# Kernel optimization log

Hardware: AMD Instinct MI355X
Metric: run time of the kernel (lower is better)

The kernel has to match this reference:

```python
import jax, jax.numpy as jnp
import numpy as np

BN_EPS = 1e-5


def sparsemax(z):
    # z: [B, D]; sparse projection onto the simplex along last axis.
    D = z.shape[-1]
    z_sorted = jnp.flip(jnp.sort(z, axis=-1), axis=-1)          # descending
    cs = jnp.cumsum(z_sorted, axis=-1)                           # cumulative sums
    k = jnp.arange(1, D + 1, dtype=z.dtype)                      # 1..D
    support = (1.0 + k * z_sorted) > cs                          # support condition
    k_star = jnp.sum(support, axis=-1, keepdims=True)            # support size, int
    cs_k = jnp.take_along_axis(cs, k_star - 1, axis=-1)
    tau = (cs_k - 1.0) / k_star.astype(z.dtype)                  # threshold
    return jnp.maximum(z - tau, 0.0)


def setup_inputs() -> dict:
    key = jax.random.key(0)
    k1, k2, k3 = jax.random.split(key, 3)
    B, D = 32768, 1024
    a = jax.random.normal(k1, (B, D), dtype=jnp.float32)
    p = jax.random.uniform(k2, (B, D), dtype=jnp.float32)        # prior scales in (0,1)
    W = jax.random.normal(k3, (D, D), dtype=jnp.float32) * (1.0 / np.sqrt(D))
    b = jnp.zeros((D,), dtype=jnp.float32)
    gamma = jnp.ones((D,), dtype=jnp.float32)
    beta = jnp.zeros((D,), dtype=jnp.float32)
    return {"a": a, "p": p, "W": W, "b": b, "gamma": gamma, "beta": beta}


def reference(a, p, W, b, gamma, beta):
    # Linear: a @ W^T + b  (torch nn.Linear convention)
    h = jnp.einsum("bd,ed->be", a, W) + b
    # BatchNorm1d (training mode: batch stats, biased variance)
    mean = jnp.mean(h, axis=0)
    var = jnp.mean(jnp.square(h - mean), axis=0)
    h = (h - mean) * jax.lax.rsqrt(var + BN_EPS) * gamma + beta
    # Prior scaling, then sparsemax -> attention mask
    mask = sparsemax(p * h)
    return mask
```

## Files before the change

### kernel.cpp

```cpp
#include <hip/hip_runtime.h>
#include <hip/hip_fp16.h>
#include <stdint.h>

typedef _Float16 f16x8 __attribute__((ext_vector_type(8)));
typedef _Float16 f16x2 __attribute__((ext_vector_type(2)));
typedef float f32x4 __attribute__((ext_vector_type(4)));

#define BM 128
#define BN 128
#define BK 64

__device__ __forceinline__ void async_copy16(const void* g, void* l) {
  __builtin_amdgcn_global_load_lds(
      (__attribute__((address_space(1))) void*)(g),
      (__attribute__((address_space(3))) void*)(l),
      16, 0, 0);
}

__global__ __launch_bounds__(256) void cvt_f32_f16_2(const float* __restrict__ inA, size_t na,
                                                     const float* __restrict__ inW, size_t nw,
                                                     _Float16* __restrict__ outA,
                                                     _Float16* __restrict__ outW) {
  size_t i = ((size_t)blockIdx.x * 256 + threadIdx.x) * 8;
  const float* in;
  _Float16* out;
  if (i < na) {
    in = inA; out = outA;
  } else {
    i -= na;
    if (i >= nw) return;
    in = inW; out = outW;
  }
  float4 u = *(const float4*)(in + i);
  float4 v = *(const float4*)(in + i + 4);
  f16x8 h;
  h[0] = (_Float16)u.x; h[1] = (_Float16)u.y; h[2] = (_Float16)u.z; h[3] = (_Float16)u.w;
  h[4] = (_Float16)v.x; h[5] = (_Float16)v.y; h[6] = (_Float16)v.z; h[7] = (_Float16)v.w;
  *(f16x8*)(out + i) = h;
}

template <bool H16>
__global__ __launch_bounds__(256) void gemm_direct(const _Float16* __restrict__ Ah,
                                                   const _Float16* __restrict__ Wh,
                                                   const float* __restrict__ bias,
                                                   void* __restrict__ Hout,
                                                   float* __restrict__ psum,
                                                   float* __restrict__ psumsq,
                                                   int M, int N, int K) {
  __shared__ __attribute__((aligned(16))) _Float16 lsA[BM * BK];
  __shared__ __attribute__((aligned(16))) _Float16 lsB[BN * BK];

  const int tid  = threadIdx.x;
  const int wave = tid >> 6;
  const int lane = tid & 63;
  const int wrow = (wave >> 1) * 64;
  const int wcol = (wave & 1) * 64;
  const int l16  = lane & 15;
  const int quad = lane >> 4;

  const int nx = gridDim.x;
  const int li = blockIdx.y * nx + blockIdx.x;
  const int xcd = li & 7;
  const int jj  = li >> 3;
  const int bnT = jj % nx;
  const int bmT = xcd + (jj / nx) * 8;
  const int bm = bmT * BM;
  const int bn = bnT * BN;

  f32x4 acc[4][4];
#pragma unroll
  for (int i = 0; i < 4; ++i)
#pragma unroll
    for (int j = 0; j < 4; ++j) acc[i][j] = (f32x4){0.f, 0.f, 0.f, 0.f};

  for (int k0 = 0; k0 < K; k0 += BK) {
#pragma unroll
    for (int i = 0; i < 4; ++i) {
      const int basechunk = i * 256 + wave * 64;
      const int g   = basechunk + lane;
      const int row = g >> 3;
      const int kc  = ((g & 7) ^ (row & 7)) << 3;
      async_copy16(Ah + (size_t)(bm + row) * K + k0 + kc, &lsA[basechunk * 8]);
      async_copy16(Wh + (size_t)(bn + row) * K + k0 + kc, &lsB[basechunk * 8]);
    }
    __syncthreads();

#pragma unroll
    for (int kk = 0; kk < BK; kk += 32) {
      f16x8 af[4], bf[4];
#pragma unroll
      for (int i = 0; i < 4; ++i) {
        const int r = wrow + i * 16 + l16;
        const int col = ((kk >> 3) + quad) ^ (l16 & 7);
        af[i] = *(const f16x8*)&lsA[r * 64 + col * 8];
      }
#pragma unroll
      for (int j = 0; j < 4; ++j) {
        const int r = wcol + j * 16 + l16;
        const int col = ((kk >> 3) + quad) ^ (l16 & 7);
        bf[j] = *(const f16x8*)&lsB[r * 64 + col * 8];
      }
#pragma unroll
      for (int i = 0; i < 4; ++i)
#pragma unroll
        for (int j = 0; j < 4; ++j)
          acc[i][j] = __builtin_amdgcn_mfma_f32_16x16x32_f16(af[i], bf[j], acc[i][j], 0, 0, 0);
    }
    __syncthreads();
  }

#pragma unroll
  for (int j = 0; j < 4; ++j) {
    const int c = bn + wcol + j * 16 + l16;
    const float bv = bias[c];
    float s = 0.f, s2 = 0.f;
#pragma unroll
    for (int i = 0; i < 4; ++i) {
      const int r = bm + wrow + i * 16 + quad * 4;
      f32x4 v = acc[i][j];
      const float v0 = v[0] + bv, v1 = v[1] + bv, v2 = v[2] + bv, v3 = v[3] + bv;
      s += v0 + v1 + v2 + v3;
      s2 += v0 * v0 + v1 * v1 + v2 * v2 + v3 * v3;
      if constexpr (H16) {
        f16x2* H2 = (f16x2*)Hout;
        const size_t d0 = (size_t)(r >> 1) * N + c;
        H2[d0]     = (f16x2){(_Float16)v0, (_Float16)v1};
        H2[d0 + N] = (f16x2){(_Float16)v2, (_Float16)v3};
      } else {
        float* Cp = (float*)Hout + (size_t)r * N + c;
        Cp[0] = v0; Cp[(size_t)N] = v1; Cp[2 * (size_t)N] = v2; Cp[3 * (size_t)N] = v3;
      }
    }
    s  += __shfl_xor(s, 16, 64);  s  += __shfl_xor(s, 32, 64);
    s2 += __shfl_xor(s2, 16, 64); s2 += __shfl_xor(s2, 32, 64);
    if (quad == 0) {
      const size_t slot = (size_t)(bmT * 2 + (wave >> 1)) * N + c;
      psum[slot] = s;
      psumsq[slot] = s2;
    }
  }
}

__global__ __launch_bounds__(256) void gemm_fallback(const float* __restrict__ Af,
                                                     const float* __restrict__ Wf,
                                                     const float* __restrict__ bias,
                                                     float* __restrict__ C,
                                                     float* __restrict__ sum,
                                                     float* __restrict__ sumsq,
                                                     int M, int N, int K) {
  __shared__ __attribute__((aligned(16))) _Float16 lsA[BM * BK];
  __shared__ __attribute__((aligned(16))) _Float16 lsB[BN * BK];
  const int tid  = threadIdx.x;
  const int wave = tid >> 6;
  const int lane = tid & 63;
  const int wrow = (wave >> 1) * 64;
  const int wcol = (wave & 1) * 64;
  const int l16  = lane & 15;
  const int quad = lane >> 4;
  const int bm = blockIdx.y * BM;
  const int bn = blockIdx.x * BN;

  f32x4 acc[4][4];
#pragma unroll
  for (int i = 0; i < 4; ++i)
#pragma unroll
    for (int j = 0; j < 4; ++j) acc[i][j] = (f32x4){0.f, 0.f, 0.f, 0.f};

  for (int k0 = 0; k0 < K; k0 += BK) {
#pragma unroll
    for (int i = 0; i < 4; ++i) {
      const int g   = i * 256 + tid;
      const int row = g >> 3;
      const int kc  = ((g & 7) ^ (row & 7)) << 3;
      {
        const float* src = Af + (size_t)(bm + row) * K + k0 + kc;
        float4 u = *(const float4*)src;
        float4 v = *(const float4*)(src + 4);
        f16x8 h;
        h[0] = (_Float16)u.x; h[1] = (_Float16)u.y; h[2] = (_Float16)u.z; h[3] = (_Float16)u.w;
        h[4] = (_Float16)v.x; h[5] = (_Float16)v.y; h[6] = (_Float16)v.z; h[7] = (_Float16)v.w;
        *(f16x8*)&lsA[g * 8] = h;
      }
      {
        const float* src = Wf + (size_t)(bn + row) * K + k0 + kc;
        float4 u = *(const float4*)src;
        float4 v = *(const float4*)(src + 4);
        f16x8 h;
        h[0] = (_Float16)u.x; h[1] = (_Float16)u.y; h[2] = (_Float16)u.z; h[3] = (_Float16)u.w;
        h[4] = (_Float16)v.x; h[5] = (_Float16)v.y; h[6] = (_Float16)v.z; h[7] = (_Float16)v.w;
        *(f16x8*)&lsB[g * 8] = h;
      }
    }
    __syncthreads();
#pragma unroll
    for (int kk = 0; kk < BK; kk += 32) {
      f16x8 af[4], bf[4];
#pragma unroll
      for (int i = 0; i < 4; ++i) {
        const int r = wrow + i * 16 + l16;
        const int col = ((kk >> 3) + quad) ^ (l16 & 7);
        af[i] = *(const f16x8*)&lsA[r * 64 + col * 8];
      }
#pragma unroll
      for (int j = 0; j < 4; ++j) {
        const int r = wcol + j * 16 + l16;
        const int col = ((kk >> 3) + quad) ^ (l16 & 7);
        bf[j] = *(const f16x8*)&lsB[r * 64 + col * 8];
      }
#pragma unroll
      for (int i = 0; i < 4; ++i)
#pragma unroll
        for (int j = 0; j < 4; ++j)
          acc[i][j] = __builtin_amdgcn_mfma_f32_16x16x32_f16(af[i], bf[j], acc[i][j], 0, 0, 0);
    }
    __syncthreads();
  }

#pragma unroll
  for (int j = 0; j < 4; ++j) {
    const int c = bn + wcol + j * 16 + l16;
    const float bv = bias[c];
    float s = 0.f, s2 = 0.f;
#pragma unroll
    for (int i = 0; i < 4; ++i) {
      const int r = bm + wrow + i * 16 + quad * 4;
      float* Cp = C + (size_t)r * N + c;
      f32x4 v = acc[i][j];
#pragma unroll
      for (int rr = 0; rr < 4; ++rr) {
        float val = v[rr] + bv;
        Cp[(size_t)rr * N] = val;
        s += val;
        s2 += val * val;
      }
    }
    s  += __shfl_xor(s, 16, 64);  s  += __shfl_xor(s, 32, 64);
    s2 += __shfl_xor(s2, 16, 64); s2 += __shfl_xor(s2, 32, 64);
    if (quad == 0) {
      atomicAdd(&sum[c], s);
      atomicAdd(&sumsq[c], s2);
    }
  }
}

__global__ __launch_bounds__(256) void bn_finalize_wave(const float* __restrict__ psum,
                                                        const float* __restrict__ psumsq,
                                                        const float* __restrict__ gamma,
                                                        const float* __restrict__ beta,
                                                        float* __restrict__ scale,
                                                        float* __restrict__ shift,
                                                        float invB, int S, int D) {
  const int wave = threadIdx.x >> 6;
  const int lane = threadIdx.x & 63;
  const int c = blockIdx.x * 4 + wave;
  float s = 0.f, q = 0.f;
  for (int u = lane; u < S; u += 64) {
    s += psum[(size_t)u * D + c];
    q += psumsq[(size_t)u * D + c];
  }
#pragma unroll
  for (int o = 32; o > 0; o >>= 1) {
    s += __shfl_xor(s, o, 64);
    q += __shfl_xor(q, o, 64);
  }
  if (lane == 0) {
    float mean = s * invB;
    float var  = q * invB - mean * mean;
    float rstd = rsqrtf(var + 1e-5f);
    float sc = rstd * gamma[c];
    scale[c] = sc;
    shift[c] = beta[c] - mean * sc;
  }
}

__global__ __launch_bounds__(256) void bn_finalize(const float* __restrict__ sum,
                                                   const float* __restrict__ sumsq,
                                                   const float* __restrict__ gamma,
                                                   const float* __restrict__ beta,
                                                   float* __restrict__ scale,
                                                   float* __restrict__ shift,
                                                   float invB) {
  const int c = blockIdx.x * 256 + threadIdx.x;
  float mean = sum[c] * invB;
  float var  = sumsq[c] * invB - mean * mean;
  float rstd = rsqrtf(var + 1e-5f);
  float sc = rstd * gamma[c];
  scale[c] = sc;
  shift[c] = beta[c] - mean * sc;
}

__global__ __launch_bounds__(256) void bn_sparsemax_h2(const _Float16* __restrict__ H2,
                                                       const float* __restrict__ P,
                                                       const float* __restrict__ scale,
                                                       const float* __restrict__ shift,
                                                       float* __restrict__ out, int D) {
  const int wave = threadIdx.x >> 6;
  const int lane = threadIdx.x & 63;
  const int row = blockIdx.x * 4 + wave;
  const int rp  = row >> 1;
  const int par = row & 1;

  const f16x8* Hc = (const f16x8*)(H2 + (size_t)rp * 2 * D);
  const f32x4* P4 = (const f32x4*)(P + (size_t)row * D);
  const f32x4* SC = (const f32x4*)scale;
  const f32x4* SH = (const f32x4*)shift;

  f32x4 z[4];
  float tot = 0.f;
#pragma unroll
  for (int j = 0; j < 4; ++j) {
    const int idx = j * 64 + lane;
    f16x8 h = Hc[idx];
    f32x4 hv = {(float)h[par], (float)h[2 + par], (float)h[4 + par], (float)h[6 + par]};
    f32x4 zz = P4[idx] * (hv * SC[idx] + SH[idx]);
    z[j] = zz;
    tot += zz[0] + zz[1] + zz[2] + zz[3];
  }
#pragma unroll
  for (int o = 32; o > 0; o >>= 1) tot += __shfl_xor(tot, o, 64);

  float tau = (tot - 1.0f) / (float)D;
  float kprev = -1.0f;
  for (int it = 0; it < 64; ++it) {
    float s = 0.f, kf = 0.f;
#pragma unroll
    for (int j = 0; j < 4; ++j)
#pragma unroll
      for (int c = 0; c < 4; ++c) {
        float zz = z[j][c];
        if (zz > tau) { s += zz; kf += 1.0f; }
      }
#pragma unroll
    for (int o = 32; o > 0; o >>= 1) {
      s  += __shfl_xor(s, o, 64);
      kf += __shfl_xor(kf, o, 64);
    }
    tau = (s - 1.0f) / kf;
    if (kf == kprev) break;
    kprev = kf;
  }

  f32x4* O4 = (f32x4*)(out + (size_t)row * D);
#pragma unroll
  for (int j = 0; j < 4; ++j) {
    const int idx = j * 64 + lane;
    f32x4 o;
#pragma unroll
    for (int c = 0; c < 4; ++c) o[c] = fmaxf(z[j][c] - tau, 0.f);
    O4[idx] = o;
  }
}

__global__ __launch_bounds__(256) void bn_sparsemax_f32(const float* __restrict__ H,
                                                        const float* __restrict__ P,
                                                        const float* __restrict__ scale,
                                                        const float* __restrict__ shift,
                                                        float* __restrict__ out, int D) {
  const int wave = threadIdx.x >> 6;
  const int lane = threadIdx.x & 63;
  const int row = blockIdx.x * 4 + wave;
  const size_t rowoff = (size_t)row * D;
  const f32x4* H4 = (const f32x4*)(H + rowoff);
  const f32x4* P4 = (const f32x4*)(P + rowoff);
  const f32x4* SC = (const f32x4*)scale;
  const f32x4* SH = (const f32x4*)shift;

  f32x4 z[4];
  float tot = 0.f;
#pragma unroll
  for (int j = 0; j < 4; ++j) {
    const int idx = j * 64 + lane;
    f32x4 zz = P4[idx] * (H4[idx] * SC[idx] + SH[idx]);
    z[j] = zz;
    tot += zz[0] + zz[1] + zz[2] + zz[3];
  }
#pragma unroll
  for (int o = 32; o > 0; o >>= 1) tot += __shfl_xor(tot, o, 64);

  float tau = (tot - 1.0f) / (float)D;
  float kprev = -1.0f;
  for (int it = 0; it < 64; ++it) {
    float s = 0.f, kf = 0.f;
#pragma unroll
    for (int j = 0; j < 4; ++j)
#pragma unroll
      for (int c = 0; c < 4; ++c) {
        float zz = z[j][c];
        if (zz > tau) { s += zz; kf += 1.0f; }
      }
#pragma unroll
    for (int o = 32; o > 0; o >>= 1) {
      s  += __shfl_xor(s, o, 64);
      kf += __shfl_xor(kf, o, 64);
    }
    tau = (s - 1.0f) / kf;
    if (kf == kprev) break;
    kprev = kf;
  }

  f32x4* O4 = (f32x4*)(out + rowoff);
#pragma unroll
  for (int j = 0; j < 4; ++j) {
    const int idx = j * 64 + lane;
    f32x4 o;
#pragma unroll
    for (int c = 0; c < 4; ++c) o[c] = fmaxf(z[j][c] - tau, 0.f);
    O4[idx] = o;
  }
}

extern "C" void kernel_launch(void* const* d_in, const int* in_sizes, int n_in,
                              void* d_out, int out_size, void* d_ws, size_t ws_size,
                              hipStream_t stream) {
  const float* a     = (const float*)d_in[0];
  const float* p     = (const float*)d_in[1];
  const float* W     = (const float*)d_in[2];
  const float* b     = (const float*)d_in[3];
  const float* gamma = (const float*)d_in[4];
  const float* beta  = (const float*)d_in[5];
  float* out = (float*)d_out;

  const int D = in_sizes[3];
  const int Brows = in_sizes[0] / D;
  const int K = D, N = D;
  const size_t na = (size_t)Brows * D;
  const size_t nw = (size_t)D * D;
  const int S = (Brows / BM) * 2;

  const size_t statsB = (size_t)D * S * sizeof(float);
  float* psum   = (float*)d_ws;
  float* psumsq = (float*)((char*)d_ws + statsB);
  float* wscale = (float*)((char*)d_ws + 2 * statsB);
  float* wshift = wscale + D;
  const size_t off_Ah = 2 * statsB + 16384;
  _Float16* Ah = (_Float16*)((char*)d_ws + off_Ah);
  _Float16* Wh = Ah + na;
  _Float16* H2 = Wh + nw;
  const size_t need1 = off_Ah + (na + nw) * sizeof(_Float16);
  const size_t need2 = need1 + na * sizeof(_Float16);

  if (ws_size >= need1) {
    cvt_f32_f16_2<<<dim3((unsigned)((na + nw) / 8 / 256)), 256, 0, stream>>>(
        a, na, W, nw, Ah, Wh);
    const bool h16 = ws_size >= need2;
    if (h16) {
      gemm_direct<true><<<dim3(N / BN, Brows / BM), 256, 0, stream>>>(
          Ah, Wh, b, H2, psum, psumsq, Brows, N, K);
    } else {
      gemm_direct<false><<<dim3(N / BN, Brows / BM), 256, 0, stream>>>(
          Ah, Wh, b, out, psum, psumsq, Brows, N, K);
    }
    bn_finalize_wave<<<dim3(D / 4), 256, 0, stream>>>(psum, psumsq, gamma, beta,
                                                      wscale, wshift,
                                                      1.0f / (float)Brows, S, D);
    if (h16) {
      bn_sparsemax_h2<<<dim3(Brows / 4), 256, 0, stream>>>(H2, p, wscale, wshift, out, D);
    } else {
      bn_sparsemax_f32<<<dim3(Brows / 4), 256, 0, stream>>>(out, p, wscale, wshift, out, D);
    }
  } else {
    float* wsum   = (float*)d_ws;
    float* wsumsq = wsum + D;
    float* fscale = wsum + 2 * D;
    float* fshift = wsum + 3 * D;
    hipMemsetAsync(d_ws, 0, 2 * D * sizeof(float), stream);
    gemm_fallback<<<dim3(N / BN, Brows / BM), 256, 0, stream>>>(
        a, W, b, out, wsum, wsumsq, Brows, N, K);
    bn_finalize<<<dim3(D / 256), 256, 0, stream>>>(wsum, wsumsq, gamma, beta, fscale, fshift,
                                                   1.0f / (float)Brows);
    bn_sparsemax_f32<<<dim3(Brows / 4), 256, 0, stream>>>(out, p, fscale, fshift, out, D);
  }
}
```

Measured before the change: 424.0 us.

## Fuse activation fp32-to-fp16 conversion into GEMM tile loads, convert only weights

The separate conversion pass over the large activation matrix is removed. The GEMM now reads fp32 activations directly, converts them in registers and stores them to the swizzled LDS layout, while weights are still pre-converted and loaded asynchronously. This avoids writing and re-reading a 64MB fp16 copy of the activations. In exchange, the activation tile loads are synchronous register round-trips instead of async global-to-LDS copies, and the GEMM reads twice the bytes for A. The fallback kernel's LDS store is also changed from a swizzled global read to a swizzled LDS write.

```diff
diff --git a/kernel.cpp b/kernel.cpp
--- a/kernel.cpp
+++ b/kernel.cpp
@@ -17,20 +17,11 @@
       16, 0, 0);
 }
 
-__global__ __launch_bounds__(256) void cvt_f32_f16_2(const float* __restrict__ inA, size_t na,
-                                                     const float* __restrict__ inW, size_t nw,
-                                                     _Float16* __restrict__ outA,
-                                                     _Float16* __restrict__ outW) {
+__global__ __launch_bounds__(256) void cvt_f32_f16(const float* __restrict__ in,
+                                                   _Float16* __restrict__ out,
+                                                   size_t n) {
   size_t i = ((size_t)blockIdx.x * 256 + threadIdx.x) * 8;
-  const float* in;
-  _Float16* out;
-  if (i < na) {
-    in = inA; out = outA;
-  } else {
-    i -= na;
-    if (i >= nw) return;
-    in = inW; out = outW;
-  }
+  if (i + 8 > n) return;
   float4 u = *(const float4*)(in + i);
   float4 v = *(const float4*)(in + i + 4);
   f16x8 h;
@@ -40,13 +31,13 @@
 }
 
 template <bool H16>
-__global__ __launch_bounds__(256) void gemm_direct(const _Float16* __restrict__ Ah,
-                                                   const _Float16* __restrict__ Wh,
-                                                   const float* __restrict__ bias,
-                                                   void* __restrict__ Hout,
-                                                   float* __restrict__ psum,
-                                                   float* __restrict__ psumsq,
-                                                   int M, int N, int K) {
+__global__ __launch_bounds__(256) void gemm_a32(const float* __restrict__ Af,
+                                                const _Float16* __restrict__ Wh,
+                                                const float* __restrict__ bias,
+                                                void* __restrict__ Hout,
+                                                float* __restrict__ psum,
+                                                float* __restrict__ psumsq,
+                                                int M, int N, int K) {
   __shared__ __attribute__((aligned(16))) _Float16 lsA[BM * BK];
   __shared__ __attribute__((aligned(16))) _Float16 lsB[BN * BK];
 
@@ -80,8 +71,21 @@
       const int g   = basechunk + lane;
       const int row = g >> 3;
       const int kc  = ((g & 7) ^ (row & 7)) << 3;
-      async_copy16(Ah + (size_t)(bm + row) * K + k0 + kc, &lsA[basechunk * 8]);
       async_copy16(Wh + (size_t)(bn + row) * K + k0 + kc, &lsB[basechunk * 8]);
+    }
+#pragma unroll
+    for (int i = 0; i < 4; ++i) {
+      const int g   = i * 256 + tid;
+      const int row = g >> 3;
+      const int kc8 = g & 7;
+      const float* src = Af + (size_t)(bm + row) * K + k0 + kc8 * 8;
+      float4 u = *(const float4*)src;
+      float4 v = *(const float4*)(src + 4);
+      f16x8 h;
+      h[0] = (_Float16)u.x; h[1] = (_Float16)u.y; h[2] = (_Float16)u.z; h[3] = (_Float16)u.w;
+      h[4] = (_Float16)v.x; h[5] = (_Float16)v.y; h[6] = (_Float16)v.z; h[7] = (_Float16)v.w;
+      const int slot = row * 8 + (kc8 ^ (row & 7));
+      *(f16x8*)&lsA[slot * 8] = h;
     }
     __syncthreads();
 
@@ -171,24 +175,25 @@
     for (int i = 0; i < 4; ++i) {
       const int g   = i * 256 + tid;
       const int row = g >> 3;
-      const int kc  = ((g & 7) ^ (row & 7)) << 3;
+      const int kc8 = g & 7;
+      const int slot = row * 8 + (kc8 ^ (row & 7));
       {
-        const float* src = Af + (size_t)(bm + row) * K + k0 + kc;
+        const float* src = Af + (size_t)(bm + row) * K + k0 + kc8 * 8;
         float4 u = *(const float4*)src;
         float4 v = *(const float4*)(src + 4);
         f16x8 h;
         h[0] = (_Float16)u.x; h[1] = (_Float16)u.y; h[2] = (_Float16)u.z; h[3] = (_Float16)u.w;
         h[4] = (_Float16)v.x; h[5] = (_Float16)v.y; h[6] = (_Float16)v.z; h[7] = (_Float16)v.w;
-        *(f16x8*)&lsA[g * 8] = h;
+        *(f16x8*)&lsA[slot * 8] = h;
       }
       {
-        const float* src = Wf + (size_t)(bn + row) * K + k0 + kc;
+        const float* src = Wf + (size_t)(bn + row) * K + k0 + kc8 * 8;
         float4 u = *(const float4*)src;
         float4 v = *(const float4*)(src + 4);
         f16x8 h;
         h[0] = (_Float16)u.x; h[1] = (_Float16)u.y; h[2] = (_Float16)u.z; h[3] = (_Float16)u.w;
         h[4] = (_Float16)v.x; h[5] = (_Float16)v.y; h[6] = (_Float16)v.z; h[7] = (_Float16)v.w;
-        *(f16x8*)&lsB[g * 8] = h;
+        *(f16x8*)&lsB[slot * 8] = h;
       }
     }
     __syncthreads();
@@ -432,32 +437,28 @@
   float* psumsq = (float*)((char*)d_ws + statsB);
   float* wscale = (float*)((char*)d_ws + 2 * statsB);
   float* wshift = wscale + D;
-  const size_t off_Ah = 2 * statsB + 16384;
-  _Float16* Ah = (_Float16*)((char*)d_ws + off_Ah);
-  _Float16* Wh = Ah + na;
+  const size_t off_Wh = 2 * statsB + 16384;
+  _Float16* Wh = (_Float16*)((char*)d_ws + off_Wh);
   _Float16* H2 = Wh + nw;
-  const size_t need1 = off_Ah + (na + nw) * sizeof(_Float16);
-  const size_t need2 = need1 + na * sizeof(_Float16);
-
-  if (ws_size >= need1) {
-    cvt_f32_f16_2<<<dim3((unsigned)((na + nw) / 8 / 256)), 256, 0, stream>>>(
-        a, na, W, nw, Ah, Wh);
-    const bool h16 = ws_size >= need2;
-    if (h16) {
-      gemm_direct<true><<<dim3(N / BN, Brows / BM), 256, 0, stream>>>(
-          Ah, Wh, b, H2, psum, psumsq, Brows, N, K);
-    } else {
-      gemm_direct<false><<<dim3(N / BN, Brows / BM), 256, 0, stream>>>(
-          Ah, Wh, b, out, psum, psumsq, Brows, N, K);
-    }
+  const size_t need_h16 = off_Wh + (nw + na) * sizeof(_Float16);
+  const size_t need_w   = off_Wh + nw * sizeof(_Float16);
+
+  if (ws_size >= need_h16) {
+    cvt_f32_f16<<<dim3((unsigned)(nw / 8 / 256)), 256, 0, stream>>>(W, Wh, nw);
+    gemm_a32<true><<<dim3(N / BN, Brows / BM), 256, 0, stream>>>(
+        a, Wh, b, H2, psum, psumsq, Brows, N, K);
     bn_finalize_wave<<<dim3(D / 4), 256, 0, stream>>>(psum, psumsq, gamma, beta,
                                                       wscale, wshift,
                                                       1.0f / (float)Brows, S, D);
-    if (h16) {
-      bn_sparsemax_h2<<<dim3(Brows / 4), 256, 0, stream>>>(H2, p, wscale, wshift, out, D);
-    } else {
-      bn_sparsemax_f32<<<dim3(Brows / 4), 256, 0, stream>>>(out, p, wscale, wshift, out, D);
-    }
+    bn_sparsemax_h2<<<dim3(Brows / 4), 256, 0, stream>>>(H2, p, wscale, wshift, out, D);
+  } else if (ws_size >= need_w) {
+    cvt_f32_f16<<<dim3((unsigned)(nw / 8 / 256)), 256, 0, stream>>>(W, Wh, nw);
+    gemm_a32<false><<<dim3(N / BN, Brows / BM), 256, 0, stream>>>(
+        a, Wh, b, out, psum, psumsq, Brows, N, K);
+    bn_finalize_wave<<<dim3(D / 4), 256, 0, stream>>>(psum, psumsq, gamma, beta,
+                                                      wscale, wshift,
+                                                      1.0f / (float)Brows, S, D);
+    bn_sparsemax_f32<<<dim3(Brows / 4), 256, 0, stream>>>(out, p, wscale, wshift, out, D);
   } else {
     float* wsum   = (float*)d_ws;
     float* wsumsq = wsum + D;
```

Result: slower. 441.5 us (+4.1%).
